# Optimization experiments

Hardware: AMD Instinct MI355X
Metric: run time of the kernel (lower is better)

The kernel has to match this reference:

```python
import jax, jax.numpy as jnp
import numpy as np

B, S, E, H = 2, 2048, 1024, 16
D = E // H  # head_dim = 64


def setup_inputs() -> dict:
    key = jax.random.key(0)
    ks = jax.random.split(key, 9)
    w = 0.02
    return {
        "values": jax.random.normal(ks[0], (B, S, E), dtype=jnp.float32),
        "keys": jax.random.normal(ks[1], (B, S, E), dtype=jnp.float32),
        "queries": jax.random.normal(ks[2], (B, S, E), dtype=jnp.float32),
        "Wv": jax.random.normal(ks[3], (E, E), dtype=jnp.float32) * w,
        "bv": jnp.zeros((E,), dtype=jnp.float32),
        "Wk": jax.random.normal(ks[4], (E, E), dtype=jnp.float32) * w,
        "bk": jnp.zeros((E,), dtype=jnp.float32),
        "Wq": jax.random.normal(ks[5], (E, E), dtype=jnp.float32) * w,
        "bq": jnp.zeros((E,), dtype=jnp.float32),
    }


def reference(values, keys, queries, Wv, bv, Wk, bk, Wq, bq):
    b = queries.shape[0]
    v_len, k_len, q_len = values.shape[1], keys.shape[1], queries.shape[1]
    # torch.nn.Linear: y = x @ W^T + b
    k = (keys @ Wk.T + bk).reshape(b, k_len, H, D)
    v = (values @ Wv.T + bv).reshape(b, v_len, H, D)
    q = (queries @ Wq.T + bq).reshape(b, q_len, H, D)
    # NOTE: faithful to source, scaling is by sqrt(q_len), not sqrt(head_dim)
    energy = jnp.einsum('bqhd,bkhd->bhqk', q, k) / jnp.sqrt(jnp.float32(q_len))
    attn = jax.nn.softmax(energy, axis=3)
    # NOTE: faithful to source einsum 'bhqk,bvhd->bqhd' (k and v summed separately)
    out = jnp.einsum('bhqk,bvhd->bqhd', attn, v)
    return out
```

## Files before the change

kernel.cpp:

```cpp
#include <hip/hip_runtime.h>


#define BB 2
#define SS 2048
#define EE 1024

constexpr int NSC = 128;
constexpr int SC  = SS / NSC;

__global__ void colsum_kernel(const float* __restrict__ values,
                              float* __restrict__ colsum) {
    const int tid = threadIdx.x;
    const int b   = blockIdx.x % BB;
    const int sc  = blockIdx.x / BB;
    const int e0  = tid * 4;
    const float* p =
        values + (size_t)b * SS * EE + (size_t)sc * SC * EE + e0;
    float a0 = 0.f, a1 = 0.f, a2 = 0.f, a3 = 0.f;
    #pragma unroll
    for (int s = 0; s < SC; ++s) {
        float4 u = *reinterpret_cast<const float4*>(p + (size_t)s * EE);
        a0 += u.x; a1 += u.y; a2 += u.z; a3 += u.w;
    }
    float* dst = colsum + b * EE + e0;
    atomicAdd(dst + 0, a0);
    atomicAdd(dst + 1, a1);
    atomicAdd(dst + 2, a2);
    atomicAdd(dst + 3, a3);
}

__global__ void matvec_kernel(const float* __restrict__ Wv,
                              const float* __restrict__ bv,
                              const float* __restrict__ colsum,
                              float* __restrict__ out_row) {
    const int gtid = blockIdx.x * blockDim.x + threadIdx.x;
    const int wave = gtid >> 6;
    const int lane = threadIdx.x & 63;
    const int b = wave / EE;
    const int j = wave % EE;
    const float* w = Wv + (size_t)j * EE;
    const float* x = colsum + b * EE;
    float acc = 0.f;
    #pragma unroll
    for (int i = 0; i < EE / 256; ++i) {
        int e = i * 256 + lane * 4;
        float4 wv = *reinterpret_cast<const float4*>(w + e);
        float4 xv = *reinterpret_cast<const float4*>(x + e);
        acc += wv.x * xv.x + wv.y * xv.y + wv.z * xv.z + wv.w * xv.w;
    }
    #pragma unroll
    for (int off = 32; off; off >>= 1) acc += __shfl_down(acc, off, 64);
    if (lane == 0)
        out_row[b * EE + j] = acc + (float)SS * bv[j];
}

__global__ void bcast_kernel(const float* __restrict__ out_row,
                             float* __restrict__ out) {
    const size_t idx = (size_t)blockIdx.x * blockDim.x + threadIdx.x;
    const size_t pos = idx * 4;
    const int e = (int)(pos & (EE - 1));
    const int b = (int)(pos / ((size_t)SS * EE));
    const float4 v = *reinterpret_cast<const float4*>(out_row + b * EE + e);
    *reinterpret_cast<float4*>(out + pos) = v;
}

extern "C" void kernel_launch(void* const* d_in, const int* in_sizes, int n_in,
                              void* d_out, int out_size, void* d_ws, size_t ws_size,
                              hipStream_t stream) {
    const float* values = (const float*)d_in[0];
    const float* Wv     = (const float*)d_in[3];
    const float* bv     = (const float*)d_in[4];
    float* out = (float*)d_out;

    float* colsum  = (float*)d_ws;
    float* out_row = colsum + BB * EE;

    hipMemsetAsync(colsum, 0, BB * EE * sizeof(float), stream);

    colsum_kernel<<<BB * NSC, 256, 0, stream>>>(values, colsum);

    matvec_kernel<<<(BB * EE) / 4, 256, 0, stream>>>(Wv, bv, colsum, out_row);

    const size_t total = (size_t)BB * SS * EE;
    bcast_kernel<<<(unsigned int)(total / 4 / 256), 256, 0, stream>>>(
        out_row, out);
}
```

Before: 123.3 us.

## Fuse colsum, matvec and broadcast into one cooperative kernel with grid syncs

Replaces the memset and three separate launches with a single cooperative kernel of 1024 blocks that uses grid-wide syncs between phases. The column sum now writes per-block partials to workspace and reduces them in a second phase instead of using atomics. The matvec and the broadcast of the output row follow inside the same kernel. This removes launch gaps and atomic contention, at the cost of three grid barriers and the extra partials buffer traffic, and it requires all 1024 blocks to be resident at once.

Result: slower. 429.7 us (+248.4%).

```diff
diff --git a/kernel.cpp b/kernel.cpp
--- a/kernel.cpp
+++ b/kernel.cpp
@@ -1,67 +1,100 @@
 #include <hip/hip_runtime.h>
+#include <hip/hip_cooperative_groups.h>
+
+namespace cg = cooperative_groups;
 
 
 #define BB 2
 #define SS 2048
 #define EE 1024
 
-constexpr int NSC = 128;
-constexpr int SC  = SS / NSC;
+constexpr int GRID = 1024;
+constexpr int BLK  = 256;
+constexpr int NSC  = GRID / BB;
+constexpr int SC   = SS / NSC;
 
-__global__ void colsum_kernel(const float* __restrict__ values,
-                              float* __restrict__ colsum) {
+__global__ void __launch_bounds__(BLK, 4) fused_kernel(
+    const float* __restrict__ values,
+    const float* __restrict__ Wv,
+    const float* __restrict__ bv,
+    float* __restrict__ out,
+    float* __restrict__ ws)
+{
+    cg::grid_group grid = cg::this_grid();
     const int tid = threadIdx.x;
-    const int b   = blockIdx.x % BB;
-    const int sc  = blockIdx.x / BB;
-    const int e0  = tid * 4;
-    const float* p =
-        values + (size_t)b * SS * EE + (size_t)sc * SC * EE + e0;
-    float a0 = 0.f, a1 = 0.f, a2 = 0.f, a3 = 0.f;
-    #pragma unroll
-    for (int s = 0; s < SC; ++s) {
-        float4 u = *reinterpret_cast<const float4*>(p + (size_t)s * EE);
-        a0 += u.x; a1 += u.y; a2 += u.z; a3 += u.w;
+    const int g   = blockIdx.x;
+
+    float* partials = ws;
+    float* colsum   = ws + (size_t)GRID * EE;
+    float* out_row  = colsum + BB * EE;
+
+    {
+        const int b  = g >> 9;
+        const int sc = g & (NSC - 1);
+        const float* p = values + (size_t)b * SS * EE
+                                + (size_t)sc * SC * EE + tid * 4;
+        float4 a = {0.f, 0.f, 0.f, 0.f};
+        #pragma unroll
+        for (int s = 0; s < SC; ++s) {
+            float4 u = *reinterpret_cast<const float4*>(p + (size_t)s * EE);
+            a.x += u.x; a.y += u.y; a.z += u.z; a.w += u.w;
+        }
+        *reinterpret_cast<float4*>(partials + (size_t)g * EE + tid * 4) = a;
     }
-    float* dst = colsum + b * EE + e0;
-    atomicAdd(dst + 0, a0);
-    atomicAdd(dst + 1, a1);
-    atomicAdd(dst + 2, a2);
-    atomicAdd(dst + 3, a3);
-}
+    grid.sync();
 
-__global__ void matvec_kernel(const float* __restrict__ Wv,
-                              const float* __restrict__ bv,
-                              const float* __restrict__ colsum,
-                              float* __restrict__ out_row) {
-    const int gtid = blockIdx.x * blockDim.x + threadIdx.x;
-    const int wave = gtid >> 6;
-    const int lane = threadIdx.x & 63;
-    const int b = wave / EE;
-    const int j = wave % EE;
-    const float* w = Wv + (size_t)j * EE;
-    const float* x = colsum + b * EE;
-    float acc = 0.f;
-    #pragma unroll
-    for (int i = 0; i < EE / 256; ++i) {
-        int e = i * 256 + lane * 4;
-        float4 wv = *reinterpret_cast<const float4*>(w + e);
-        float4 xv = *reinterpret_cast<const float4*>(x + e);
-        acc += wv.x * xv.x + wv.y * xv.y + wv.z * xv.z + wv.w * xv.w;
+    {
+        const int t = g * BLK + tid;
+        if (t < BB * EE) {
+            const int b = t >> 10;
+            const int e = t & (EE - 1);
+            const float* pp = partials + (size_t)b * NSC * EE + e;
+            float s0 = 0.f, s1 = 0.f, s2 = 0.f, s3 = 0.f;
+            #pragma unroll 4
+            for (int sc = 0; sc < NSC; sc += 4) {
+                s0 += pp[(size_t)(sc + 0) * EE];
+                s1 += pp[(size_t)(sc + 1) * EE];
+                s2 += pp[(size_t)(sc + 2) * EE];
+                s3 += pp[(size_t)(sc + 3) * EE];
+            }
+            colsum[t] = (s0 + s1) + (s2 + s3);
+        }
     }
-    #pragma unroll
-    for (int off = 32; off; off >>= 1) acc += __shfl_down(acc, off, 64);
-    if (lane == 0)
-        out_row[b * EE + j] = acc + (float)SS * bv[j];
-}
+    grid.sync();
 
-__global__ void bcast_kernel(const float* __restrict__ out_row,
-                             float* __restrict__ out) {
-    const size_t idx = (size_t)blockIdx.x * blockDim.x + threadIdx.x;
-    const size_t pos = idx * 4;
-    const int e = (int)(pos & (EE - 1));
-    const int b = (int)(pos / ((size_t)SS * EE));
-    const float4 v = *reinterpret_cast<const float4*>(out_row + b * EE + e);
-    *reinterpret_cast<float4*>(out + pos) = v;
+    {
+        const int w    = (g * BLK + tid) >> 6;
+        const int lane = tid & 63;
+        if (w < BB * EE) {
+            const int b = w >> 10;
+            const int j = w & (EE - 1);
+            const float* wr = Wv + (size_t)j * EE;
+            const float* x  = colsum + b * EE;
+            float acc = 0.f;
+            #pragma unroll
+            for (int i = 0; i < EE / 256; ++i) {
+                int e = i * 256 + lane * 4;
+                float4 wv = *reinterpret_cast<const float4*>(wr + e);
+                float4 xv = *reinterpret_cast<const float4*>(x + e);
+                acc += wv.x * xv.x + wv.y * xv.y + wv.z * xv.z + wv.w * xv.w;
+            }
+            #pragma unroll
+            for (int off = 32; off; off >>= 1) acc += __shfl_down(acc, off, 64);
+            if (lane == 0) out_row[w] = acc + (float)SS * bv[j];
+        }
+    }
+    grid.sync();
+
+    {
+        const size_t base = (size_t)g * ((size_t)BB * SS * EE / GRID);
+        const int b = (int)(base >> 21);
+        const float4 v =
+            *reinterpret_cast<const float4*>(out_row + b * EE + tid * 4);
+        float* o = out + base;
+        #pragma unroll
+        for (int i = 0; i < 4; ++i)
+            *reinterpret_cast<float4*>(o + (size_t)i * 1024 + tid * 4) = v;
+    }
 }
 
 extern "C" void kernel_launch(void* const* d_in, const int* in_sizes, int n_in,
@@ -71,17 +104,10 @@
     const float* Wv     = (const float*)d_in[3];
     const float* bv     = (const float*)d_in[4];
     float* out = (float*)d_out;
+    float* ws  = (float*)d_ws;
 
-    float* colsum  = (float*)d_ws;
-    float* out_row = colsum + BB * EE;
-
-    hipMemsetAsync(colsum, 0, BB * EE * sizeof(float), stream);
-
-    colsum_kernel<<<BB * NSC, 256, 0, stream>>>(values, colsum);
-
-    matvec_kernel<<<(BB * EE) / 4, 256, 0, stream>>>(Wv, bv, colsum, out_row);
-
-    const size_t total = (size_t)BB * SS * EE;
-    bcast_kernel<<<(unsigned int)(total / 4 / 256), 256, 0, stream>>>(
-        out_row, out);
+    void* args[] = { (void*)&values, (void*)&Wv, (void*)&bv,
+                     (void*)&out, (void*)&ws };
+    hipLaunchCooperativeKernel((void*)fused_kernel, dim3(GRID), dim3(BLK),
+                               args, 0, stream);
 }
```
